# Optimization experiments

Hardware: AMD Instinct MI355X
Metric: run time of the kernel (lower is better)

Reference implementation:

```python
import jax, jax.numpy as jnp
import numpy as np

B, O, M, H, E = 32, 64, 128, 4, 64  # batch, num_obj, memory_len, heads, embed


def setup_inputs() -> dict:
    key = jax.random.key(0)
    ks = jax.random.split(key, 10)
    s = 1.0 / np.sqrt(E)
    return {
        "query": jax.random.normal(ks[0], (B, O, E), jnp.float32),
        "context": jax.random.normal(ks[1], (B, M, E), jnp.float32),
        "memory": jax.random.normal(ks[2], (B, M, E), jnp.float32),
        "W_ch": jax.random.normal(ks[3], (E, H * E), jnp.float32) * s,
        "b_ch": jax.random.normal(ks[4], (H * E,), jnp.float32) * s,
        "w_logit": jax.random.normal(ks[5], (E,), jnp.float32) * s,
        "b_logit": jax.random.normal(ks[6], (1,), jnp.float32) * s,
        "W_rh": jax.random.normal(ks[7], (H * E, E), jnp.float32) * (1.0 / np.sqrt(H * E)),
        "b_rh": jax.random.normal(ks[8], (E,), jnp.float32) * (1.0 / np.sqrt(H * E)),
        "temp": jnp.float32(1.0),
    }


def reference(query, context, memory, W_ch, b_ch, w_logit, b_logit, W_rh, b_rh, temp):
    # create heads: [B,O,E] -> [B,O,H,E]
    q = (query @ W_ch + b_ch).reshape(B, O, H, E)
    # broadcast add query heads and context over memory axis: [B,O,M,H,E]
    qc = jnp.tanh(context[:, None, :, None, :] + q[:, :, None, :, :])
    # logit projection -> [B,O,M,H]
    logits = jnp.einsum("bomhe,e->bomh", qc, w_logit) + b_logit[0]
    # softmax over memory axis (dim=2)
    probs = jax.nn.softmax(logits / temp, axis=2)
    # weighted sum of memory over M: [B,O,H,E]
    heads = jnp.einsum("bomh,bme->bohe", probs, memory)
    heads = jax.nn.leaky_relu(heads, negative_slope=0.01)
    out = heads.reshape(B, O, H * E) @ W_rh + b_rh
    return out
```

## Files before the change

### kernel.cpp

```cpp
#include <hip/hip_runtime.h>
#include <hip/hip_fp16.h>

#define B 32
#define O 64
#define M 128
#define H 4
#define E 64
#define SC 2.88539008177792681f
#define LOG2E 1.44269504088896341f

#if __has_builtin(__builtin_amdgcn_exp2f)
#define EXP2F(x) __builtin_amdgcn_exp2f(x)
#else
#define EXP2F(x) __exp2f(x)
#endif

__device__ __forceinline__ float rl(float v, int lane) {
    return __uint_as_float(__builtin_amdgcn_readlane(__float_as_uint(v), lane));
}
__device__ __forceinline__ unsigned pk2h(float a, float b) {
    return (unsigned)__half_as_ushort(__float2half_rn(a)) |
           ((unsigned)__half_as_ushort(__float2half_rn(b)) << 16);
}

__global__ __launch_bounds__(256) void prep_kernel(
    const float* __restrict__ query, const float* __restrict__ context,
    const float* __restrict__ memory, const float* __restrict__ W_ch,
    const float* __restrict__ b_ch,
    __half* __restrict__ ctx_T, __half* __restrict__ mem_h, float* __restrict__ q_all)
{
    __shared__ float s[128 * 68];
    const int t = threadIdx.x, blk = blockIdx.x;

    if (blk < 32) {
        const int b = blk;
        const float* ctx = context + b * (M * E);
        #pragma unroll
        for (int i = 0; i < 8; ++i) {
            int idx = i * 1024 + t * 4;
            float4 v = *(const float4*)(ctx + idx);
            int m = idx >> 6, e = idx & 63;
            *(float4*)(&s[m * 68 + e]) = v;
        }
        {
            const float* mem = memory + b * (M * E);
            __half* mh = mem_h + (size_t)b * (M * E);
            #pragma unroll
            for (int i = 0; i < 8; ++i) {
                int idx = i * 1024 + t * 4;
                float4 v = *(const float4*)(mem + idx);
                *(uint2*)(mh + idx) = make_uint2(pk2h(v.x, v.y), pk2h(v.z, v.w));
            }
        }
        __syncthreads();
        {
            int e = t >> 2, mb = (t & 3) * 32;
            uint4 o[4];
            #pragma unroll
            for (int qd = 0; qd < 4; ++qd) {
                unsigned u[4];
                #pragma unroll
                for (int k = 0; k < 4; ++k) {
                    int m0 = mb + qd * 8 + 2 * k;
                    u[k] = pk2h(s[m0 * 68 + e] * SC, s[(m0 + 1) * 68 + e] * SC);
                }
                o[qd] = make_uint4(u[0], u[1], u[2], u[3]);
            }
            uint4* dst = (uint4*)(ctx_T + (size_t)b * (E * M) + e * M + mb);
            dst[0] = o[0]; dst[1] = o[1]; dst[2] = o[2]; dst[3] = o[3];
        }
    } else {
        const int r0 = (blk - 32) * 4;
        s[t] = query[(r0 + (t & 3)) * 64 + (t >> 2)];
        __syncthreads();
        float bc = b_ch[t];
        float a0 = bc, a1 = bc, a2 = bc, a3 = bc;
        #pragma unroll 8
        for (int k = 0; k < 64; ++k) {
            float4 qv = *(const float4*)(&s[k * 4]);
            float wv = W_ch[k * 256 + t];
            a0 = fmaf(qv.x, wv, a0);
            a1 = fmaf(qv.y, wv, a1);
            a2 = fmaf(qv.z, wv, a2);
            a3 = fmaf(qv.w, wv, a3);
        }
        float* qa = q_all + (size_t)r0 * 256 + t;
        qa[0] = a0 * SC; qa[256] = a1 * SC; qa[512] = a2 * SC; qa[768] = a3 * SC;
    }
}

__global__ __launch_bounds__(256) void attn_main(
    const __half* __restrict__ ctx_T, const __half* __restrict__ mem_h,
    const float* __restrict__ q_all, const float* __restrict__ w_logit,
    const float* __restrict__ b_logit, const float* __restrict__ temp,
    __half* __restrict__ heads_h)
{
    __shared__ __half s_ctx[E * M];
    __shared__ float  s_prob[M * H];
    __shared__ float  s_part[H * 4 * E];

    const int t = threadIdx.x, lane = t & 63, w = t >> 6;
    const int bo = blockIdx.x, b = bo >> 6;

    {
        const uint4* g1 = (const uint4*)(ctx_T + (size_t)b * (E * M));
        uint4* l1 = (uint4*)s_ctx;
        #pragma unroll
        for (int p = 0; p < 4; ++p)
            l1[p * 256 + t] = g1[p * 256 + t];
    }
    float qv  = q_all[bo * 256 + t];
    float wl  = w_logit[lane];
    float we2 = 2.0f * wl;
    float sumw = wl;
    #pragma unroll
    for (int sft = 1; sft < 64; sft <<= 1) sumw += __shfl_xor(sumw, sft);
    const float bl  = b_logit[0];
    const float lsc = LOG2E / temp[0];
    __syncthreads();

    float acc0 = 0.f, acc1 = 0.f;
    const __half2* c2p = (const __half2*)s_ctx;
    #pragma unroll 8
    for (int e = 0; e < 64; ++e) {
        float2 cf = __half22float2(c2p[e * 64 + lane]);
        float qe = rl(qv, e);
        float w2 = rl(we2, e);
        float r0 = __builtin_amdgcn_rcpf(1.0f + EXP2F(cf.x + qe));
        float r1 = __builtin_amdgcn_rcpf(1.0f + EXP2F(cf.y + qe));
        acc0 = fmaf(w2, r0, acc0);
        acc1 = fmaf(w2, r1, acc1);
    }
    float l0 = (sumw - acc0 + bl) * lsc;
    float l1 = (sumw - acc1 + bl) * lsc;
    float mx = fmaxf(l0, l1);
    #pragma unroll
    for (int sft = 1; sft < 64; sft <<= 1) mx = fmaxf(mx, __shfl_xor(mx, sft));
    float e0 = EXP2F(l0 - mx);
    float e1 = EXP2F(l1 - mx);
    float sum = e0 + e1;
    #pragma unroll
    for (int sft = 1; sft < 64; sft <<= 1) sum += __shfl_xor(sum, sft);
    float rs = __builtin_amdgcn_rcpf(sum);
    s_prob[(2 * lane) * H + w]     = e0 * rs;
    s_prob[(2 * lane + 1) * H + w] = e1 * rs;
    __syncthreads();

    float h0 = 0.f, h1 = 0.f, h2 = 0.f, h3 = 0.f;
    {
        const __half* mem = mem_h + (size_t)b * (M * E) + lane;
        #pragma unroll 8
        for (int i = 0; i < 32; ++i) {
            int m = 32 * w + i;
            float4 p = *(const float4*)(&s_prob[m * 4]);
            float mv = __half2float(mem[m * 64]);
            h0 = fmaf(p.x, mv, h0);
            h1 = fmaf(p.y, mv, h1);
            h2 = fmaf(p.z, mv, h2);
            h3 = fmaf(p.w, mv, h3);
        }
    }
    s_part[0 * 256 + w * 64 + lane] = h0;
    s_part[1 * 256 + w * 64 + lane] = h1;
    s_part[2 * 256 + w * 64 + lane] = h2;
    s_part[3 * 256 + w * 64 + lane] = h3;
    __syncthreads();
    float hv = s_part[w * 256 + lane] + s_part[w * 256 + 64 + lane]
             + s_part[w * 256 + 128 + lane] + s_part[w * 256 + 192 + lane];
    hv = (hv > 0.f) ? hv : 0.01f * hv;
    heads_h[(size_t)bo * 256 + t] = __float2half_rn(hv);
}

__global__ __launch_bounds__(256) void post_kernel(
    const __half* __restrict__ heads_h, const float* __restrict__ W_rh,
    const float* __restrict__ b_rh, float* __restrict__ out)
{
    __shared__ __half s_h[4 * 256];
    const int t = threadIdx.x, lane = t & 63, r = t >> 6;
    const int r0 = blockIdx.x * 4;
    ((uint4*)s_h)[t & 127] = ((const uint4*)(heads_h + (size_t)r0 * 256))[t & 127];
    __syncthreads();
    const __half2* hr = (const __half2*)(s_h + r * 256);
    const float* Wp = W_rh + lane;
    float acc = 0.f;
    #pragma unroll 8
    for (int jp = 0; jp < 128; ++jp) {
        float2 hh = __half22float2(hr[jp]);
        acc = fmaf(hh.x, Wp[(2 * jp) * 64], acc);
        acc = fmaf(hh.y, Wp[(2 * jp + 1) * 64], acc);
    }
    out[(size_t)(r0 + r) * 64 + lane] = acc + b_rh[lane];
}

extern "C" void kernel_launch(void* const* d_in, const int* in_sizes, int n_in,
                              void* d_out, int out_size, void* d_ws, size_t ws_size,
                              hipStream_t stream) {
    const float* query   = (const float*)d_in[0];
    const float* context = (const float*)d_in[1];
    const float* memory  = (const float*)d_in[2];
    const float* W_ch    = (const float*)d_in[3];
    const float* b_ch    = (const float*)d_in[4];
    const float* w_logit = (const float*)d_in[5];
    const float* b_logit = (const float*)d_in[6];
    const float* W_rh    = (const float*)d_in[7];
    const float* b_rh    = (const float*)d_in[8];
    const float* temp    = (const float*)d_in[9];
    float* out = (float*)d_out;

    __half* ctx_T   = (__half*)d_ws;
    __half* mem_h   = ctx_T + (size_t)B * E * M;
    float*  q_all   = (float*)(mem_h + (size_t)B * M * E);
    __half* heads_h = (__half*)(q_all + (size_t)B * O * H * E);

    prep_kernel<<<544, 256, 0, stream>>>(query, context, memory, W_ch, b_ch,
                                         ctx_T, mem_h, q_all);
    attn_main<<<B * O, 256, 0, stream>>>(ctx_T, mem_h, q_all, w_logit,
                                         b_logit, temp, heads_h);
    post_kernel<<<512, 256, 0, stream>>>(heads_h, W_rh, b_rh, out);
}
```

Before: 107.2 us.

## Factor tanh exponentials into precomputed exp(context) and exp(query) products

The exponentials of the scaled context and query-head values are now computed once in the prep kernel, so the inner attention loop forms exp(c+q) as a product instead of calling exp2 per element. Two reciprocals are merged into one by inverting the product a0*a1 and recovering each term with a multiply. Context is stored in fp32 rather than fp16, which doubles the shared-memory staging size and global traffic for that tensor. This risks overflow or inf for large inputs, since exp of the scaled values is no longer bounded by the sum inside the exponent.

```diff
diff --git a/kernel.cpp b/kernel.cpp
--- a/kernel.cpp
+++ b/kernel.cpp
@@ -27,7 +27,7 @@
     const float* __restrict__ query, const float* __restrict__ context,
     const float* __restrict__ memory, const float* __restrict__ W_ch,
     const float* __restrict__ b_ch,
-    __half* __restrict__ ctx_T, __half* __restrict__ mem_h, float* __restrict__ q_all)
+    float* __restrict__ ctx_E, __half* __restrict__ mem_h, float* __restrict__ q_E)
 {
     __shared__ float s[128 * 68];
     const int t = threadIdx.x, blk = blockIdx.x;
@@ -55,19 +55,16 @@
         __syncthreads();
         {
             int e = t >> 2, mb = (t & 3) * 32;
-            uint4 o[4];
+            float4* dst = (float4*)(ctx_E + (size_t)b * (E * M) + e * M + mb);
             #pragma unroll
-            for (int qd = 0; qd < 4; ++qd) {
-                unsigned u[4];
-                #pragma unroll
-                for (int k = 0; k < 4; ++k) {
-                    int m0 = mb + qd * 8 + 2 * k;
-                    u[k] = pk2h(s[m0 * 68 + e] * SC, s[(m0 + 1) * 68 + e] * SC);
-                }
-                o[qd] = make_uint4(u[0], u[1], u[2], u[3]);
+            for (int i = 0; i < 8; ++i) {
+                float4 v;
+                v.x = EXP2F(SC * s[(mb + 4 * i + 0) * 68 + e]);
+                v.y = EXP2F(SC * s[(mb + 4 * i + 1) * 68 + e]);
+                v.z = EXP2F(SC * s[(mb + 4 * i + 2) * 68 + e]);
+                v.w = EXP2F(SC * s[(mb + 4 * i + 3) * 68 + e]);
+                dst[i] = v;
             }
-            uint4* dst = (uint4*)(ctx_T + (size_t)b * (E * M) + e * M + mb);
-            dst[0] = o[0]; dst[1] = o[1]; dst[2] = o[2]; dst[3] = o[3];
         }
     } else {
         const int r0 = (blk - 32) * 4;
@@ -84,55 +81,61 @@
             a2 = fmaf(qv.z, wv, a2);
             a3 = fmaf(qv.w, wv, a3);
         }
-        float* qa = q_all + (size_t)r0 * 256 + t;
-        qa[0] = a0 * SC; qa[256] = a1 * SC; qa[512] = a2 * SC; qa[768] = a3 * SC;
+        float* qa = q_E + (size_t)r0 * 256 + t;
+        qa[0]   = EXP2F(SC * a0);
+        qa[256] = EXP2F(SC * a1);
+        qa[512] = EXP2F(SC * a2);
+        qa[768] = EXP2F(SC * a3);
     }
 }
 
 __global__ __launch_bounds__(256) void attn_main(
-    const __half* __restrict__ ctx_T, const __half* __restrict__ mem_h,
-    const float* __restrict__ q_all, const float* __restrict__ w_logit,
+    const float* __restrict__ ctx_E, const __half* __restrict__ mem_h,
+    const float* __restrict__ q_E, const float* __restrict__ w_logit,
     const float* __restrict__ b_logit, const float* __restrict__ temp,
     __half* __restrict__ heads_h)
 {
-    __shared__ __half s_ctx[E * M];
-    __shared__ float  s_prob[M * H];
-    __shared__ float  s_part[H * 4 * E];
+    __shared__ float s_E[E * M];
+    __shared__ float s_prob[M * H];
+    __shared__ float s_part[H * 4 * E];
 
     const int t = threadIdx.x, lane = t & 63, w = t >> 6;
     const int bo = blockIdx.x, b = bo >> 6;
 
     {
-        const uint4* g1 = (const uint4*)(ctx_T + (size_t)b * (E * M));
-        uint4* l1 = (uint4*)s_ctx;
+        const uint4* g1 = (const uint4*)(ctx_E + (size_t)b * (E * M));
+        uint4* l1 = (uint4*)s_E;
         #pragma unroll
-        for (int p = 0; p < 4; ++p)
+        for (int p = 0; p < 8; ++p)
             l1[p * 256 + t] = g1[p * 256 + t];
     }
-    float qv  = q_all[bo * 256 + t];
-    float wl  = w_logit[lane];
-    float we2 = 2.0f * wl;
+    const float qE = q_E[bo * 256 + t];
+    const float wl = w_logit[lane];
     float sumw = wl;
     #pragma unroll
     for (int sft = 1; sft < 64; sft <<= 1) sumw += __shfl_xor(sumw, sft);
     const float bl  = b_logit[0];
     const float lsc = LOG2E / temp[0];
+    const float base = (sumw + bl) * lsc;
+    const float lsc2 = -2.0f * lsc;
     __syncthreads();
 
     float acc0 = 0.f, acc1 = 0.f;
-    const __half2* c2p = (const __half2*)s_ctx;
+    const float2* Ep = (const float2*)s_E;
     #pragma unroll 8
     for (int e = 0; e < 64; ++e) {
-        float2 cf = __half22float2(c2p[e * 64 + lane]);
-        float qe = rl(qv, e);
-        float w2 = rl(we2, e);
-        float r0 = __builtin_amdgcn_rcpf(1.0f + EXP2F(cf.x + qe));
-        float r1 = __builtin_amdgcn_rcpf(1.0f + EXP2F(cf.y + qe));
-        acc0 = fmaf(w2, r0, acc0);
-        acc1 = fmaf(w2, r1, acc1);
-    }
-    float l0 = (sumw - acc0 + bl) * lsc;
-    float l1 = (sumw - acc1 + bl) * lsc;
+        float2 Ec = Ep[e * 64 + lane];
+        float Eq = rl(qE, e);
+        float we = rl(wl, e);
+        float a0 = fmaf(Ec.x, Eq, 1.0f);
+        float a1 = fmaf(Ec.y, Eq, 1.0f);
+        float r  = __builtin_amdgcn_rcpf(a0 * a1);
+        acc0 = fmaf(we, a1 * r, acc0);
+        acc1 = fmaf(we, a0 * r, acc1);
+    }
+
+    float l0 = fmaf(lsc2, acc0, base);
+    float l1 = fmaf(lsc2, acc1, base);
     float mx = fmaxf(l0, l1);
     #pragma unroll
     for (int sft = 1; sft < 64; sft <<= 1) mx = fmaxf(mx, __shfl_xor(mx, sft));
@@ -207,14 +210,14 @@
     const float* temp    = (const float*)d_in[9];
     float* out = (float*)d_out;
 
-    __half* ctx_T   = (__half*)d_ws;
-    __half* mem_h   = ctx_T + (size_t)B * E * M;
-    float*  q_all   = (float*)(mem_h + (size_t)B * M * E);
-    __half* heads_h = (__half*)(q_all + (size_t)B * O * H * E);
+    float*  ctx_E   = (float*)d_ws;
+    __half* mem_h   = (__half*)(ctx_E + (size_t)B * E * M);
+    float*  q_E     = (float*)(mem_h + (size_t)B * M * E);
+    __half* heads_h = (__half*)(q_E + (size_t)B * O * 256);
 
     prep_kernel<<<544, 256, 0, stream>>>(query, context, memory, W_ch, b_ch,
-                                         ctx_T, mem_h, q_all);
-    attn_main<<<B * O, 256, 0, stream>>>(ctx_T, mem_h, q_all, w_logit,
+                                         ctx_E, mem_h, q_E);
+    attn_main<<<B * O, 256, 0, stream>>>(ctx_E, mem_h, q_E, w_logit,
                                          b_logit, temp, heads_h);
     post_kernel<<<512, 256, 0, stream>>>(heads_h, W_rh, b_rh, out);
 }
```

After: 102.0 us. 1.05x faster.
